# Optimization experiments

Measured on AMD Instinct MI355X. Metric: run time of the kernel, lower is better.

Reference implementation:

```python
import jax, jax.numpy as jnp
import numpy as np

B, N, T, F_IN, F_OUT = 4, 2048, 12, 32, 32
ALPHA = 0.2  # leaky relu negative slope
NEG_INF = -9e15


def setup_inputs() -> dict:
    key = jax.random.key(0)
    k = jax.random.split(key, 6)
    x = jax.random.normal(k[0], (B, N, T, F_IN), dtype=jnp.float32)
    adj = jax.random.randint(k[1], (N, N), 0, 2, dtype=jnp.int32)
    W = jax.random.normal(k[2], (T * F_IN, T * F_OUT), dtype=jnp.float32) * 0.05
    a = jax.random.normal(k[3], (2 * T * F_OUT, 1), dtype=jnp.float32) * 0.05
    conv_w = jax.random.normal(k[4], (T, T, 3), dtype=jnp.float32) * 0.1  # (out_ch, in_ch, k)
    conv_b = jnp.zeros((T,), dtype=jnp.float32)
    return {"x": x, "adj": adj, "W": W, "a": a, "conv_w": conv_w, "conv_b": conv_b}


def reference(x, adj, W, a, conv_w, conv_b):
    Bz, Nn, Tt, Fi = x.shape
    Fo = W.shape[1] // Tt
    # temporal conv: channels = timesteps, length = nodes*features
    xt = x.transpose(0, 2, 1, 3).reshape(Bz, Tt, Nn * Fi)  # (B,T,L)
    xt = jax.lax.conv_general_dilated(
        xt, conv_w, window_strides=(1,), padding=[(1, 1)],
        dimension_numbers=("NCH", "OIH", "NCH")) + conv_b[None, :, None]
    xt = xt.reshape(Bz, Tt, Nn, Fi).transpose(0, 2, 1, 3).reshape(Bz, Nn, Tt * Fi)
    Wh = xt @ W  # (B, N, T*Fo)
    # e[b,i,j] = leakyrelu(Wh[b,i].a1 + Wh[b,j].a2)  -- avoids O(N^2 * 2F) concat
    a1 = a[: Tt * Fo, 0]
    a2 = a[Tt * Fo:, 0]
    f1 = Wh @ a1  # (B, N)
    f2 = Wh @ a2  # (B, N)
    e = jax.nn.leaky_relu(f1[:, :, None] + f2[:, None, :], negative_slope=ALPHA)
    e = jnp.where(adj[None, :, :] > 0, e, NEG_INF)
    attn = jax.nn.softmax(e, axis=-1)  # (B, N, N); dropout omitted (eval mode)
    h_prime = attn @ Wh  # (B, N, T*Fo)
    return jax.nn.elu(h_prime).reshape(Bz, Nn, Tt, Fo)
```

## Files before the change

kernel.cpp:

```cpp
#include <hip/hip_runtime.h>

using short8 = __attribute__((ext_vector_type(8))) short;
using f32x4  = __attribute__((ext_vector_type(4))) float;
using f32x16 = __attribute__((ext_vector_type(16))) float;

__device__ __forceinline__ unsigned short f2bf(float f) {
  unsigned u = __float_as_uint(f);
  u += 0x7fffu + ((u >> 16) & 1u);
  return (unsigned short)(u >> 16);
}

__global__ __launch_bounds__(256) void pack_w_kernel(const float* __restrict__ W,
                                                     unsigned short* __restrict__ wtp) {
  const int f = blockIdx.x * 4 + (threadIdx.x >> 6);
  const int l = threadIdx.x & 63;
  const int kk = f / 24, ct = f % 24;
  const int il = l & 15, kg = l >> 4;
  const float* src = W + (size_t)(kk * 32 + kg * 8) * 384 + ct * 16 + il;
  short8 v;
#pragma unroll
  for (int e = 0; e < 8; ++e) v[e] = (short)f2bf(src[(size_t)e * 384]);
  *reinterpret_cast<short8*>((char*)wtp + ((size_t)f << 10) + l * 16) = v;
}

__global__ __launch_bounds__(256) void adjmask_kernel(const int* __restrict__ adj,
                                                      unsigned* __restrict__ adjm,
                                                      float* __restrict__ f12) {
  if (blockIdx.x < 64) f12[blockIdx.x * 256 + threadIdx.x] = 0.f;
  const int wv = (blockIdx.x << 2) + (threadIdx.x >> 6);
  const int lane = threadIdx.x & 63;
  const int row = wv >> 5, j0 = (wv & 31) << 6;
  unsigned long long mask = __ballot(adj[(size_t)row * 2048 + j0 + lane] > 0);
  if (lane == 0) {
    adjm[row * 64 + (j0 >> 5)]     = (unsigned)mask;
    adjm[row * 64 + (j0 >> 5) + 1] = (unsigned)(mask >> 32);
  }
}

__global__ __launch_bounds__(256) void gemm_wh5_kernel(const float* __restrict__ x,
                                                       const float* __restrict__ cw,
                                                       const float* __restrict__ cb,
                                                       const unsigned short* __restrict__ wtp,
                                                       const float* __restrict__ a,
                                                       unsigned short* __restrict__ whp,
                                                       float* __restrict__ f1,
                                                       float* __restrict__ f2) {
  __shared__ __align__(16) char lds[24768 + 6400 + 1792];
  float* xin = (float*)lds;
  unsigned short* atile = (unsigned short*)lds;
  unsigned short* wtile = (unsigned short*)(lds + 24768);
  float* cws = (float*)(lds + 24768 + 6400);
  float* cbs = cws + 432;

  const int tid = threadIdx.x;
  const int rb = blockIdx.x;
  const int b = rb >> 8;
  const int jg2 = (rb >> 1) & 127;
  const int ch2 = rb & 1;
  const int r0 = ((b << 7) + jg2) << 4;
  const int w = tid >> 6, lane = tid & 63;
  const int il = lane & 15, kg = lane >> 4;

  for (int i = tid; i < 432; i += 256) cws[i] = cw[i];
  if (tid < 12) cbs[tid] = cb[tid];
  const float* xb = x + (size_t)b * 2048 * 12 * 32;
#pragma unroll
  for (int t = 0; t < 12; ++t) {
    for (int i = tid; i < 514; i += 256) {
      const int gp = jg2 * 512 + i - 1;
      float v = 0.f;
      if ((unsigned)gp < 65536u) v = xb[((size_t)(gp >> 5) * 12 + t) * 32 + (gp & 31)];
      xin[t * 516 + i] = v;
    }
  }
  __syncthreads();

  const int ploc = tid * 2;
  float accv0[12], accv1[12];
#pragma unroll
  for (int to = 0; to < 12; ++to) { accv0[to] = cbs[to]; accv1[to] = cbs[to]; }
#pragma unroll
  for (int ti = 0; ti < 12; ++ti) {
    const float x0 = xin[ti * 516 + ploc];
    const float x1 = xin[ti * 516 + ploc + 1];
    const float x2 = xin[ti * 516 + ploc + 2];
    const float x3 = xin[ti * 516 + ploc + 3];
#pragma unroll
    for (int to = 0; to < 12; ++to) {
      const float* wp = &cws[(to * 12 + ti) * 3];
      const float w0 = wp[0], w1 = wp[1], w2 = wp[2];
      accv0[to] += x0 * w0 + x1 * w1 + x2 * w2;
      accv1[to] += x1 * w0 + x2 * w1 + x3 * w2;
    }
  }
  __syncthreads();

  {
    const int row = ploc >> 5, f = ploc & 31;
    unsigned* ap32 = (unsigned*)(atile + row * 392 + f);
#pragma unroll
    for (int to = 0; to < 12; ++to) {
      const unsigned lo = f2bf(accv0[to]), hi = f2bf(accv1[to]);
      ap32[to * 16] = lo | (hi << 16);
    }
  }
  __syncthreads();

  f32x4 acc[3];
#pragma unroll
  for (int t = 0; t < 3; ++t) acc[t] = (f32x4){0.f, 0.f, 0.f, 0.f};
  const unsigned short* arow = atile + il * 392 + kg * 8;
  const int ct0 = ch2 * 12 + w * 3;
  const char* wb = (const char*)wtp + ((size_t)ct0 << 10) + lane * 16;

  short8 bcur[3], bnxt[3];
#pragma unroll
  for (int t = 0; t < 3; ++t)
    bcur[t] = *reinterpret_cast<const short8*>(wb + ((size_t)t << 10));
#pragma unroll
  for (int kk = 0; kk < 12; ++kk) {
    if (kk < 11) {
#pragma unroll
      for (int t = 0; t < 3; ++t)
        bnxt[t] = *reinterpret_cast<const short8*>(wb + (((size_t)(kk + 1) * 24 + t) << 10));
    }
    short8 af = *reinterpret_cast<const short8*>(arow + kk * 32);
#pragma unroll
    for (int t = 0; t < 3; ++t)
      acc[t] = __builtin_amdgcn_mfma_f32_16x16x32_bf16(af, bcur[t], acc[t], 0, 0, 0);
#pragma unroll
    for (int t = 0; t < 3; ++t) bcur[t] = bnxt[t];
  }

  float p1[4] = {0.f, 0.f, 0.f, 0.f}, p2[4] = {0.f, 0.f, 0.f, 0.f};
#pragma unroll
  for (int t = 0; t < 3; ++t) {
    const int c = (ct0 + t) * 16 + il;
    const float a1v = a[c], a2v = a[384 + c];
#pragma unroll
    for (int r = 0; r < 4; ++r) { p1[r] += acc[t][r] * a1v; p2[r] += acc[t][r] * a2v; }
  }
#pragma unroll
  for (int off = 1; off < 16; off <<= 1) {
#pragma unroll
    for (int r = 0; r < 4; ++r) { p1[r] += __shfl_xor(p1[r], off); p2[r] += __shfl_xor(p2[r], off); }
  }
  if (il == 0) {
#pragma unroll
    for (int r = 0; r < 4; ++r) {
      atomicAdd(&f1[r0 + kg * 4 + r], p1[r]);
      atomicAdd(&f2[r0 + kg * 4 + r], p2[r]);
    }
  }
#pragma unroll
  for (int t = 0; t < 3; ++t)
#pragma unroll
    for (int r = 0; r < 4; ++r)
      wtile[(kg * 4 + r) * 200 + (w * 3 + t) * 16 + il] = f2bf(acc[t][r]);
  __syncthreads();

#pragma unroll
  for (int rep = 0; rep < 2; ++rep) {
    const int flat = rep * 256 + tid;
    if (flat < 384) {
      const int ct32l = flat >> 6, l = flat & 63;
      const int l5 = l & 31, hw2 = l >> 5;
      short8 v;
#pragma unroll
      for (int e = 0; e < 8; ++e)
        v[e] = (short)wtile[(hw2 * 8 + e) * 200 + ct32l * 32 + l5];
      const int ct32g = ch2 * 6 + ct32l;
      *reinterpret_cast<short8*>((char*)whp +
          ((((size_t)b * 128 + jg2) * 12 + ct32g) << 10) + l * 16) = v;
    }
  }
}

__global__ __launch_bounds__(256) void f2max_kernel(const float* __restrict__ f2,
                                                    float* __restrict__ gmax) {
  __shared__ float wm[4];
  const int b = blockIdx.x;
  const int tid = threadIdx.x;
  float m = -3.0e38f;
  for (int i = tid; i < 2048; i += 256) m = fmaxf(m, f2[b * 2048 + i]);
#pragma unroll
  for (int off = 32; off; off >>= 1) m = fmaxf(m, __shfl_xor(m, off));
  if ((tid & 63) == 0) wm[tid >> 6] = m;
  __syncthreads();
  if (tid == 0) gmax[b] = fmaxf(fmaxf(wm[0], wm[1]), fmaxf(wm[2], wm[3]));
}

__global__ __launch_bounds__(256, 3) void attn13_kernel(const float* __restrict__ f1,
                                                        const float* __restrict__ f2,
                                                        const unsigned* __restrict__ adjm,
                                                        const unsigned short* __restrict__ whp,
                                                        const float* __restrict__ gmax,
                                                        float* __restrict__ out) {
  __shared__ float red[4][32][64];
  __shared__ float dred[128];
  const int bi = blockIdx.x;
  const int combo = bi % 12;
  const int b  = combo & 3;
  const int ch = combo >> 2;
  const int i0 = (bi / 12) << 5;
  const int tid = threadIdx.x;
  const int ks = tid >> 6;
  const int lane = tid & 63;
  const int l5 = lane & 31, hw = lane >> 5;
  const int hw8 = hw * 8;
  const int ig = i0 + l5;

  const unsigned* adjr = adjm + (size_t)ig * 64 + ks * 16;
  const float* f2b = f2 + b * 2048 + ks * 512 + hw8;
  const char* pbase = (const char*)whp +
      ((((size_t)b * 128 + ks * 32) * 12 + ch * 4) << 10) + lane * 16;

  const float f1v = f1[b * 2048 + ig];
  const float gm = gmax[b];
  const float mz = f1v + gm;
  const float m  = fmaxf(mz, 0.2f * mz);
  const float Az = f1v - m;
  const float Bz = 0.2f * f1v - m;

  const f32x16 zero16 = {0.f,0.f,0.f,0.f,0.f,0.f,0.f,0.f,0.f,0.f,0.f,0.f,0.f,0.f,0.f,0.f};
  f32x16 acc[4];
#pragma unroll
  for (int t = 0; t < 4; ++t) acc[t] = zero16;
  float denom = 0.f;

  short8 bA[4], bB[4];
  float4 fA0, fA1, fB0, fB1;
  unsigned wC, wN;

#define LOADB(AR, KK)                                                                   \
  { _Pragma("unroll")                                                                   \
    for (int tt = 0; tt < 4; ++tt)                                                      \
      AR[tt] = *reinterpret_cast<const short8*>(pbase + (size_t)(KK) * 12288 +          \
                                                (size_t)tt * 1024); }

#define PEL(GV, BIT, DST)                                                               \
  { const float z_ = Az + (GV);                                                         \
    const float e_ = fmaxf(z_, fmaf((GV), 0.2f, Bz));                                   \
    DST = ((bits_ >> (BIT)) & 1u) ? __expf(e_) : 0.f; }

#define PKBF(HI, LO) (((__float_as_uint(HI) + 0x8000u) & 0xffff0000u) |                 \
                      ((__float_as_uint(LO) + 0x8000u) >> 16))

#define STEPD(AR, F0, F1, SH, KK, DL)                                                   \
  { const unsigned bits_ = wC >> ((SH) + hw8);                                          \
    float p0_, p1_, p2_, p3_, p4_, p5_, p6_, p7_;                                       \
    PEL(F0.x, 0, p0_)  PEL(F0.y, 1, p1_)  PEL(F0.z, 2, p2_)  PEL(F0.w, 3, p3_)          \
    PEL(F1.x, 4, p4_)  PEL(F1.y, 5, p5_)  PEL(F1.z, 6, p6_)  PEL(F1.w, 7, p7_)          \
    denom += (((p0_ + p1_) + (p2_ + p3_)) + ((p4_ + p5_) + (p6_ + p7_)));               \
    union { unsigned u[4]; short8 s8; } cc;                                             \
    cc.u[0] = PKBF(p1_, p0_); cc.u[1] = PKBF(p3_, p2_);                                 \
    cc.u[2] = PKBF(p5_, p4_); cc.u[3] = PKBF(p7_, p6_);                                 \
    _Pragma("unroll")                                                                   \
    for (int tt = 0; tt < 4; ++tt)                                                      \
      acc[tt] = __builtin_amdgcn_mfma_f32_32x32x16_bf16(cc.s8, AR[tt], acc[tt], 0, 0, 0); \
    if (DL) {                                                                           \
      LOADB(AR, (KK) + 2)                                                               \
      const float* fp_ = f2b + ((KK) + 2) * 16;                                         \
      F0 = *reinterpret_cast<const float4*>(fp_);                                       \
      F1 = *reinterpret_cast<const float4*>(fp_ + 4);                                   \
    } }

  LOADB(bA, 0) LOADB(bB, 1)
  fA0 = *reinterpret_cast<const float4*>(f2b);
  fA1 = *reinterpret_cast<const float4*>(f2b + 4);
  fB0 = *reinterpret_cast<const float4*>(f2b + 16);
  fB1 = *reinterpret_cast<const float4*>(f2b + 20);
  wC = adjr[0];
  wN = adjr[1];

  for (int t = 0; t < 16; ++t) {
    STEPD(bA, fA0, fA1, 0, 2 * t, (t < 15))
    STEPD(bB, fB0, fB1, 16, 2 * t + 1, (t < 15))
    wC = wN;
    wN = adjr[(t + 2 < 16) ? t + 2 : 15];
  }
#undef LOADB
#undef PEL
#undef PKBF
#undef STEPD

  float dn = denom + __shfl_xor(denom, 32);
  if (hw == 0) dred[ks * 32 + l5] = dn;

#pragma unroll
  for (int r = 0; r < 2; ++r) {
#pragma unroll
    for (int tt = 0; tt < 2; ++tt) {
#pragma unroll
      for (int q = 0; q < 16; ++q) {
        const int row = (q & 3) + 8 * (q >> 2) + 4 * hw;
        red[ks][row][tt * 32 + l5] = acc[r * 2 + tt][q];
      }
    }
    __syncthreads();
    const size_t ob = ((size_t)b * 2048 + i0) * 384 + ch * 128 + r * 64;
#pragma unroll
    for (int p = 0; p < 8; ++p) {
      const int idx = p * 256 + tid;
      const int row = idx >> 6;
      const int c = idx & 63;
      float v = red[0][row][c] + red[1][row][c] + red[2][row][c] + red[3][row][c];
      const float d = dred[row] + dred[32 + row] + dred[64 + row] + dred[96 + row];
      v /= d;
      v = v > 0.f ? v : expm1f(v);
      out[ob + (size_t)row * 384 + c] = v;
    }
    __syncthreads();
  }
}

extern "C" void kernel_launch(void* const* d_in, const int* in_sizes, int n_in,
                              void* d_out, int out_size, void* d_ws, size_t ws_size,
                              hipStream_t stream) {
  const float* x  = (const float*)d_in[0];
  const int* adj  = (const int*)d_in[1];
  const float* W  = (const float*)d_in[2];
  const float* a  = (const float*)d_in[3];
  const float* cw = (const float*)d_in[4];
  const float* cb = (const float*)d_in[5];
  float* out = (float*)d_out;

  char* ws = (char*)d_ws;
  unsigned short* wtp = (unsigned short*)ws; ws += (size_t)147456 * 2;
  unsigned short* whp = (unsigned short*)ws; ws += (size_t)3145728 * 2;
  float* f1           = (float*)ws;          ws += (size_t)8192 * 4;
  float* f2           = (float*)ws;          ws += (size_t)8192 * 4;
  unsigned* adjm      = (unsigned*)ws;       ws += (size_t)2048 * 64 * 4;
  float* gmax         = (float*)ws;          ws += 64;

  pack_w_kernel<<<dim3(72), 256, 0, stream>>>(W, wtp);
  adjmask_kernel<<<dim3(16384), 256, 0, stream>>>(adj, adjm, f1);
  gemm_wh5_kernel<<<dim3(1024), 256, 0, stream>>>(x, cw, cb, wtp, a, whp, f1, f2);
  f2max_kernel<<<dim3(4), 256, 0, stream>>>(f2, gmax);
  attn13_kernel<<<dim3(768), 256, 0, stream>>>(f1, f2, adjm, whp, gmax, out);
}
```

Before: 79.79 us.

## Split attention into probability-generation kernel and pure MFMA aggregation kernel

Attention probabilities were recomputed three times, once per channel chunk, inside the MFMA loop. They are now computed once by a new pgen kernel, which writes bf16 probabilities in MFMA operand layout to a 32 MB workspace and accumulates the row denominators with atomics. The aggregation kernel then only streams the P and Wh operands into MFMAs. This removes the redundant exp work and the ALU work interleaved with matrix ops, but adds a large extra HBM write and read of the P matrix plus one more kernel launch.

```diff
diff --git a/kernel.cpp b/kernel.cpp
--- a/kernel.cpp
+++ b/kernel.cpp
@@ -25,8 +25,10 @@
 
 __global__ __launch_bounds__(256) void adjmask_kernel(const int* __restrict__ adj,
                                                       unsigned* __restrict__ adjm,
-                                                      float* __restrict__ f12) {
+                                                      float* __restrict__ f12,
+                                                      float* __restrict__ dsum) {
   if (blockIdx.x < 64) f12[blockIdx.x * 256 + threadIdx.x] = 0.f;
+  else if (blockIdx.x < 96) dsum[(blockIdx.x - 64) * 256 + threadIdx.x] = 0.f;
   const int wv = (blockIdx.x << 2) + (threadIdx.x >> 6);
   const int lane = threadIdx.x & 63;
   const int row = wv >> 5, j0 = (wv & 31) << 6;
@@ -190,30 +192,24 @@
   if (tid == 0) gmax[b] = fmaxf(fmaxf(wm[0], wm[1]), fmaxf(wm[2], wm[3]));
 }
 
-__global__ __launch_bounds__(256, 3) void attn13_kernel(const float* __restrict__ f1,
-                                                        const float* __restrict__ f2,
-                                                        const unsigned* __restrict__ adjm,
-                                                        const unsigned short* __restrict__ whp,
-                                                        const float* __restrict__ gmax,
-                                                        float* __restrict__ out) {
-  __shared__ float red[4][32][64];
-  __shared__ float dred[128];
+__global__ __launch_bounds__(256) void pgen_kernel(const float* __restrict__ f1,
+                                                   const float* __restrict__ f2,
+                                                   const unsigned* __restrict__ adjm,
+                                                   const float* __restrict__ gmax,
+                                                   unsigned short* __restrict__ php,
+                                                   float* __restrict__ dsum) {
+  __shared__ float ds[32];
   const int bi = blockIdx.x;
-  const int combo = bi % 12;
-  const int b  = combo & 3;
-  const int ch = combo >> 2;
-  const int i0 = (bi / 12) << 5;
+  const int b = bi >> 9;
+  const int rg = (bi >> 3) & 63;
+  const int jc = bi & 7;
   const int tid = threadIdx.x;
-  const int ks = tid >> 6;
-  const int lane = tid & 63;
+  const int wv = tid >> 6, lane = tid & 63;
   const int l5 = lane & 31, hw = lane >> 5;
   const int hw8 = hw * 8;
-  const int ig = i0 + l5;
-
-  const unsigned* adjr = adjm + (size_t)ig * 64 + ks * 16;
-  const float* f2b = f2 + b * 2048 + ks * 512 + hw8;
-  const char* pbase = (const char*)whp +
-      ((((size_t)b * 128 + ks * 32) * 12 + ch * 4) << 10) + lane * 16;
+  const int ig = rg * 32 + l5;
+  if (tid < 32) ds[tid] = 0.f;
+  __syncthreads();
 
   const float f1v = f1[b * 2048 + ig];
   const float gm = gmax[b];
@@ -221,72 +217,86 @@
   const float m  = fmaxf(mz, 0.2f * mz);
   const float Az = f1v - m;
   const float Bz = 0.2f * f1v - m;
+  const float* f2b = f2 + b * 2048;
+  const unsigned* adjrow = adjm + (size_t)ig * 64;
+  char* phpb = (char*)php + ((((size_t)b * 64 + rg) * 128) << 10) + lane * 16;
+
+  float dloc = 0.f;
+#pragma unroll
+  for (int s = 0; s < 4; ++s) {
+    const int js = jc * 16 + wv * 4 + s;
+    const int j0 = js * 16;
+    const float* fp = f2b + j0 + hw8;
+    const float4 g0 = *reinterpret_cast<const float4*>(fp);
+    const float4 g1 = *reinterpret_cast<const float4*>(fp + 4);
+    const unsigned word = adjrow[j0 >> 5];
+    const unsigned bits = word >> ((j0 & 16) + hw8);
+    const float gv[8] = {g0.x, g0.y, g0.z, g0.w, g1.x, g1.y, g1.z, g1.w};
+    union { unsigned short s[8]; short8 s8; } v;
+#pragma unroll
+    for (int e = 0; e < 8; ++e) {
+      const float z = Az + gv[e];
+      const float ee = fmaxf(z, fmaf(gv[e], 0.2f, Bz));
+      const float p = ((bits >> e) & 1u) ? __expf(ee) : 0.f;
+      dloc += p;
+      v.s[e] = (unsigned short)((__float_as_uint(p) + 0x8000u) >> 16);
+    }
+    *reinterpret_cast<short8*>(phpb + ((size_t)js << 10)) = v.s8;
+  }
+  atomicAdd(&ds[l5], dloc);
+  __syncthreads();
+  if (tid < 32) atomicAdd(&dsum[b * 2048 + rg * 32 + tid], ds[tid]);
+}
+
+__global__ __launch_bounds__(256, 3) void attn14_kernel(const unsigned short* __restrict__ php,
+                                                        const unsigned short* __restrict__ whp,
+                                                        const float* __restrict__ dsum,
+                                                        float* __restrict__ out) {
+  __shared__ float red[4][32][64];
+  const int bi = blockIdx.x;
+  const int combo = bi % 12;
+  const int b  = combo & 3;
+  const int ch = combo >> 2;
+  const int rg = bi / 12;
+  const int i0 = rg << 5;
+  const int tid = threadIdx.x;
+  const int ks = tid >> 6;
+  const int lane = tid & 63;
+  const int l5 = lane & 31, hw = lane >> 5;
+
+  const char* abase = (const char*)php +
+      ((((size_t)b * 64 + rg) * 128 + ks * 32) << 10) + lane * 16;
+  const char* pbase = (const char*)whp +
+      ((((size_t)b * 128 + ks * 32) * 12 + ch * 4) << 10) + lane * 16;
 
   const f32x16 zero16 = {0.f,0.f,0.f,0.f,0.f,0.f,0.f,0.f,0.f,0.f,0.f,0.f,0.f,0.f,0.f,0.f};
   f32x16 acc[4];
 #pragma unroll
   for (int t = 0; t < 4; ++t) acc[t] = zero16;
-  float denom = 0.f;
-
-  short8 bA[4], bB[4];
-  float4 fA0, fA1, fB0, fB1;
-  unsigned wC, wN;
-
-#define LOADB(AR, KK)                                                                   \
-  { _Pragma("unroll")                                                                   \
-    for (int tt = 0; tt < 4; ++tt)                                                      \
-      AR[tt] = *reinterpret_cast<const short8*>(pbase + (size_t)(KK) * 12288 +          \
-                                                (size_t)tt * 1024); }
-
-#define PEL(GV, BIT, DST)                                                               \
-  { const float z_ = Az + (GV);                                                         \
-    const float e_ = fmaxf(z_, fmaf((GV), 0.2f, Bz));                                   \
-    DST = ((bits_ >> (BIT)) & 1u) ? __expf(e_) : 0.f; }
-
-#define PKBF(HI, LO) (((__float_as_uint(HI) + 0x8000u) & 0xffff0000u) |                 \
-                      ((__float_as_uint(LO) + 0x8000u) >> 16))
-
-#define STEPD(AR, F0, F1, SH, KK, DL)                                                   \
-  { const unsigned bits_ = wC >> ((SH) + hw8);                                          \
-    float p0_, p1_, p2_, p3_, p4_, p5_, p6_, p7_;                                       \
-    PEL(F0.x, 0, p0_)  PEL(F0.y, 1, p1_)  PEL(F0.z, 2, p2_)  PEL(F0.w, 3, p3_)          \
-    PEL(F1.x, 4, p4_)  PEL(F1.y, 5, p5_)  PEL(F1.z, 6, p6_)  PEL(F1.w, 7, p7_)          \
-    denom += (((p0_ + p1_) + (p2_ + p3_)) + ((p4_ + p5_) + (p6_ + p7_)));               \
-    union { unsigned u[4]; short8 s8; } cc;                                             \
-    cc.u[0] = PKBF(p1_, p0_); cc.u[1] = PKBF(p3_, p2_);                                 \
-    cc.u[2] = PKBF(p5_, p4_); cc.u[3] = PKBF(p7_, p6_);                                 \
+
+  short8 aA, aB, bA[4], bB[4];
+
+#define LOADAB(AS, BR, KK)                                                              \
+  { AS = *reinterpret_cast<const short8*>(abase + ((size_t)(KK) << 10));                \
     _Pragma("unroll")                                                                   \
     for (int tt = 0; tt < 4; ++tt)                                                      \
-      acc[tt] = __builtin_amdgcn_mfma_f32_32x32x16_bf16(cc.s8, AR[tt], acc[tt], 0, 0, 0); \
-    if (DL) {                                                                           \
-      LOADB(AR, (KK) + 2)                                                               \
-      const float* fp_ = f2b + ((KK) + 2) * 16;                                         \
-      F0 = *reinterpret_cast<const float4*>(fp_);                                       \
-      F1 = *reinterpret_cast<const float4*>(fp_ + 4);                                   \
-    } }
-
-  LOADB(bA, 0) LOADB(bB, 1)
-  fA0 = *reinterpret_cast<const float4*>(f2b);
-  fA1 = *reinterpret_cast<const float4*>(f2b + 4);
-  fB0 = *reinterpret_cast<const float4*>(f2b + 16);
-  fB1 = *reinterpret_cast<const float4*>(f2b + 20);
-  wC = adjr[0];
-  wN = adjr[1];
-
+      BR[tt] = *reinterpret_cast<const short8*>(pbase + (size_t)(KK) * 12288 +          \
+                                                (size_t)tt * 1024); }
+
+  LOADAB(aA, bA, 0) LOADAB(aB, bB, 1)
   for (int t = 0; t < 16; ++t) {
-    STEPD(bA, fA0, fA1, 0, 2 * t, (t < 15))
-    STEPD(bB, fB0, fB1, 16, 2 * t + 1, (t < 15))
-    wC = wN;
-    wN = adjr[(t + 2 < 16) ? t + 2 : 15];
-  }
-#undef LOADB
-#undef PEL
-#undef PKBF
-#undef STEPD
-
-  float dn = denom + __shfl_xor(denom, 32);
-  if (hw == 0) dred[ks * 32 + l5] = dn;
-
+#pragma unroll
+    for (int tt = 0; tt < 4; ++tt)
+      acc[tt] = __builtin_amdgcn_mfma_f32_32x32x16_bf16(aA, bA[tt], acc[tt], 0, 0, 0);
+    if (t < 15) LOADAB(aA, bA, 2 * t + 2)
+#pragma unroll
+    for (int tt = 0; tt < 4; ++tt)
+      acc[tt] = __builtin_amdgcn_mfma_f32_32x32x16_bf16(aB, bB[tt], acc[tt], 0, 0, 0);
+    if (t < 15) LOADAB(aB, bB, 2 * t + 3)
+  }
+#undef LOADAB
+
+  const float* dsb = dsum + b * 2048 + i0;
 #pragma unroll
   for (int r = 0; r < 2; ++r) {
 #pragma unroll
@@ -305,8 +315,7 @@
       const int row = idx >> 6;
       const int c = idx & 63;
       float v = red[0][row][c] + red[1][row][c] + red[2][row][c] + red[3][row][c];
-      const float d = dred[row] + dred[32 + row] + dred[64 + row] + dred[96 + row];
-      v /= d;
+      v /= dsb[row];
       v = v > 0.f ? v : expm1f(v);
       out[ob + (size_t)row * 384 + c] = v;
     }
@@ -328,14 +337,17 @@
   char* ws = (char*)d_ws;
   unsigned short* wtp = (unsigned short*)ws; ws += (size_t)147456 * 2;
   unsigned short* whp = (unsigned short*)ws; ws += (size_t)3145728 * 2;
+  unsigned short* php = (unsigned short*)ws; ws += (size_t)16777216 * 2;
   float* f1           = (float*)ws;          ws += (size_t)8192 * 4;
   float* f2           = (float*)ws;          ws += (size_t)8192 * 4;
+  float* dsum         = (float*)ws;          ws += (size_t)8192 * 4;
   unsigned* adjm      = (unsigned*)ws;       ws += (size_t)2048 * 64 * 4;
   float* gmax         = (float*)ws;          ws += 64;
 
   pack_w_kernel<<<dim3(72), 256, 0, stream>>>(W, wtp);
-  adjmask_kernel<<<dim3(16384), 256, 0, stream>>>(adj, adjm, f1);
+  adjmask_kernel<<<dim3(16384), 256, 0, stream>>>(adj, adjm, f1, dsum);
   gemm_wh5_kernel<<<dim3(1024), 256, 0, stream>>>(x, cw, cb, wtp, a, whp, f1, f2);
   f2max_kernel<<<dim3(4), 256, 0, stream>>>(f2, gmax);
-  attn13_kernel<<<dim3(768), 256, 0, stream>>>(f1, f2, adjm, whp, gmax, out);
-}
+  pgen_kernel<<<dim3(2048), 256, 0, stream>>>(f1, f2, adjm, gmax, php, dsum);
+  attn14_kernel<<<dim3(768), 256, 0, stream>>>(php, whp, dsum, out);
+}
```

Result: slower. 83.90 us (+5.1%).

## Factor attention exponentials into per-node tables and restructure attention with LDS-staged P

Applied to the files above, without the earlier changes.

Rewrites exp(leakyrelu(f1+f2)-m) as a product of per-row and per-column exponentials, with the per-column exp(f2) and exp(0.2*f2) precomputed once as packed bf16 in f2max_kernel. This removes the per-element exp from the attention inner loop. The attention kernel now uses 512-thread blocks, each covering all output channels for 32 rows, and 16x16x32 MFMAs whose P operand is staged through double-buffered LDS. The Wh pack layout in the GEMM epilogue is reshaped to match. This avoids the cross-wave split-K reduction but adds a barrier per step, bf16 rounding of the exp table, and a branch selection per element.

```diff
diff --git a/kernel.cpp b/kernel.cpp
--- a/kernel.cpp
+++ b/kernel.cpp
@@ -2,7 +2,6 @@
 
 using short8 = __attribute__((ext_vector_type(8))) short;
 using f32x4  = __attribute__((ext_vector_type(4))) float;
-using f32x16 = __attribute__((ext_vector_type(16))) float;
 
 __device__ __forceinline__ unsigned short f2bf(float f) {
   unsigned u = __float_as_uint(f);
@@ -159,30 +158,42 @@
       wtile[(kg * 4 + r) * 200 + (w * 3 + t) * 16 + il] = f2bf(acc[t][r]);
   __syncthreads();
 
+  const int js = jg2 >> 1;
+  const int lbase = (jg2 & 1) * 32;
 #pragma unroll
   for (int rep = 0; rep < 2; ++rep) {
     const int flat = rep * 256 + tid;
     if (flat < 384) {
-      const int ct32l = flat >> 6, l = flat & 63;
-      const int l5 = l & 31, hw2 = l >> 5;
+      const int ctl = flat >> 5;
+      const int ll = flat & 31;
+      const int l_g = lbase + ll;
       short8 v;
 #pragma unroll
-      for (int e = 0; e < 8; ++e)
-        v[e] = (short)wtile[(hw2 * 8 + e) * 200 + ct32l * 32 + l5];
-      const int ct32g = ch2 * 6 + ct32l;
+      for (int e = 0; e < 8; ++e) {
+        const int jrow = (ll >> 4) * 8 + e;
+        v[e] = (short)wtile[jrow * 200 + ctl * 16 + (ll & 15)];
+      }
+      const int ctg = ch2 * 12 + ctl;
       *reinterpret_cast<short8*>((char*)whp +
-          ((((size_t)b * 128 + jg2) * 12 + ct32g) << 10) + l * 16) = v;
+          ((((size_t)b * 64 + js) * 24 + ctg) << 10) + l_g * 16) = v;
     }
   }
 }
 
 __global__ __launch_bounds__(256) void f2max_kernel(const float* __restrict__ f2,
-                                                    float* __restrict__ gmax) {
+                                                    float* __restrict__ gmax,
+                                                    unsigned* __restrict__ etab) {
   __shared__ float wm[4];
   const int b = blockIdx.x;
   const int tid = threadIdx.x;
   float m = -3.0e38f;
-  for (int i = tid; i < 2048; i += 256) m = fmaxf(m, f2[b * 2048 + i]);
+  for (int i = tid; i < 2048; i += 256) {
+    const float v = f2[b * 2048 + i];
+    m = fmaxf(m, v);
+    const unsigned e2 = f2bf(__expf(v));
+    const unsigned q2 = f2bf(__expf(0.2f * v));
+    etab[b * 2048 + i] = (e2 << 16) | q2;
+  }
 #pragma unroll
   for (int off = 32; off; off >>= 1) m = fmaxf(m, __shfl_xor(m, off));
   if ((tid & 63) == 0) wm[tid >> 6] = m;
@@ -190,127 +201,112 @@
   if (tid == 0) gmax[b] = fmaxf(fmaxf(wm[0], wm[1]), fmaxf(wm[2], wm[3]));
 }
 
-__global__ __launch_bounds__(256, 3) void attn13_kernel(const float* __restrict__ f1,
-                                                        const float* __restrict__ f2,
+__global__ __launch_bounds__(512, 4) void attn15_kernel(const float* __restrict__ f1,
+                                                        const unsigned* __restrict__ etab,
                                                         const unsigned* __restrict__ adjm,
                                                         const unsigned short* __restrict__ whp,
                                                         const float* __restrict__ gmax,
                                                         float* __restrict__ out) {
-  __shared__ float red[4][32][64];
-  __shared__ float dred[128];
+  __shared__ __align__(16) char plds[4096 + 128];
+  float* drows = (float*)(plds + 4096);
   const int bi = blockIdx.x;
-  const int combo = bi % 12;
-  const int b  = combo & 3;
-  const int ch = combo >> 2;
-  const int i0 = (bi / 12) << 5;
+  const int b = bi >> 6, rg = bi & 63;
   const int tid = threadIdx.x;
-  const int ks = tid >> 6;
-  const int lane = tid & 63;
-  const int l5 = lane & 31, hw = lane >> 5;
-  const int hw8 = hw * 8;
-  const int ig = i0 + l5;
-
-  const unsigned* adjr = adjm + (size_t)ig * 64 + ks * 16;
-  const float* f2b = f2 + b * 2048 + ks * 512 + hw8;
-  const char* pbase = (const char*)whp +
-      ((((size_t)b * 128 + ks * 32) * 12 + ch * 4) << 10) + lane * 16;
-
-  const float f1v = f1[b * 2048 + ig];
+  const int w = tid >> 6, lam = tid & 63;
+  const int h = tid >> 8;
+  const int q = w & 3;
+  const int mrem = tid & 255;
+  const int lp = mrem >> 2, pair = mrem & 3;
+  const int rowp = h * 16 + (lp & 15);
+  const int igp = rg * 32 + rowp;
+  const int jin = (lp >> 4) * 8 + pair * 2;
+
+  if (tid < 32) drows[tid] = 0.f;
+
+  const float f1v = f1[b * 2048 + igp];
   const float gm = gmax[b];
   const float mz = f1v + gm;
-  const float m  = fmaxf(mz, 0.2f * mz);
-  const float Az = f1v - m;
-  const float Bz = 0.2f * f1v - m;
-
-  const f32x16 zero16 = {0.f,0.f,0.f,0.f,0.f,0.f,0.f,0.f,0.f,0.f,0.f,0.f,0.f,0.f,0.f,0.f};
-  f32x16 acc[4];
-#pragma unroll
-  for (int t = 0; t < 4; ++t) acc[t] = zero16;
-  float denom = 0.f;
-
-  short8 bA[4], bB[4];
-  float4 fA0, fA1, fB0, fB1;
-  unsigned wC, wN;
-
-#define LOADB(AR, KK)                                                                   \
+  const float mm = fmaxf(mz, 0.2f * mz);
+  const float E1 = __expf(f1v - mm);
+  const float F1 = __expf(0.2f * f1v - mm);
+  const float T  = __expf(-f1v);
+  const unsigned* adjr = adjm + (size_t)igp * 64;
+  const unsigned* etb = etab + b * 2048;
+  char* pwr = plds + h * 1024 + lp * 16 + pair * 4;
+  const char* prd = plds + h * 1024 + lam * 16;
+  const char* wbase = (const char*)whp + ((((size_t)b * 64) * 24 + q * 6) << 10) + lam * 16;
+
+  float dloc = 0.f;
+  f32x4 acc[6];
+#pragma unroll
+  for (int t = 0; t < 6; ++t) acc[t] = (f32x4){0.f, 0.f, 0.f, 0.f};
+
+#define PGEN(BUF, S)                                                                    \
+  { const unsigned bits_ = adjr[S] >> jin;                                              \
+    const uint2 tt_ = *reinterpret_cast<const uint2*>(etb + (S) * 32 + jin);            \
+    const float e2a_ = __uint_as_float(tt_.x & 0xffff0000u);                            \
+    const float q2a_ = __uint_as_float(tt_.x << 16);                                    \
+    const bool pa_ = e2a_ > T;                                                          \
+    float va_ = (pa_ ? e2a_ : q2a_) * (pa_ ? E1 : F1);                                  \
+    va_ = (bits_ & 1u) ? va_ : 0.f;                                                     \
+    const float e2b_ = __uint_as_float(tt_.y & 0xffff0000u);                            \
+    const float q2b_ = __uint_as_float(tt_.y << 16);                                    \
+    const bool pb_ = e2b_ > T;                                                          \
+    float vb_ = (pb_ ? e2b_ : q2b_) * (pb_ ? E1 : F1);                                  \
+    vb_ = (bits_ & 2u) ? vb_ : 0.f;                                                     \
+    dloc += va_ + vb_;                                                                  \
+    const unsigned pk_ = ((__float_as_uint(vb_) + 0x8000u) & 0xffff0000u) |             \
+                         ((__float_as_uint(va_) + 0x8000u) >> 16);                      \
+    *reinterpret_cast<unsigned*>(pwr + (BUF) * 2048) = pk_; }
+
+#define LOADB(AR, S)                                                                    \
   { _Pragma("unroll")                                                                   \
-    for (int tt = 0; tt < 4; ++tt)                                                      \
-      AR[tt] = *reinterpret_cast<const short8*>(pbase + (size_t)(KK) * 12288 +          \
-                                                (size_t)tt * 1024); }
-
-#define PEL(GV, BIT, DST)                                                               \
-  { const float z_ = Az + (GV);                                                         \
-    const float e_ = fmaxf(z_, fmaf((GV), 0.2f, Bz));                                   \
-    DST = ((bits_ >> (BIT)) & 1u) ? __expf(e_) : 0.f; }
-
-#define PKBF(HI, LO) (((__float_as_uint(HI) + 0x8000u) & 0xffff0000u) |                 \
-                      ((__float_as_uint(LO) + 0x8000u) >> 16))
-
-#define STEPD(AR, F0, F1, SH, KK, DL)                                                   \
-  { const unsigned bits_ = wC >> ((SH) + hw8);                                          \
-    float p0_, p1_, p2_, p3_, p4_, p5_, p6_, p7_;                                       \
-    PEL(F0.x, 0, p0_)  PEL(F0.y, 1, p1_)  PEL(F0.z, 2, p2_)  PEL(F0.w, 3, p3_)          \
-    PEL(F1.x, 4, p4_)  PEL(F1.y, 5, p5_)  PEL(F1.z, 6, p6_)  PEL(F1.w, 7, p7_)          \
-    denom += (((p0_ + p1_) + (p2_ + p3_)) + ((p4_ + p5_) + (p6_ + p7_)));               \
-    union { unsigned u[4]; short8 s8; } cc;                                             \
-    cc.u[0] = PKBF(p1_, p0_); cc.u[1] = PKBF(p3_, p2_);                                 \
-    cc.u[2] = PKBF(p5_, p4_); cc.u[3] = PKBF(p7_, p6_);                                 \
-    _Pragma("unroll")                                                                   \
-    for (int tt = 0; tt < 4; ++tt)                                                      \
-      acc[tt] = __builtin_amdgcn_mfma_f32_32x32x16_bf16(cc.s8, AR[tt], acc[tt], 0, 0, 0); \
-    if (DL) {                                                                           \
-      LOADB(AR, (KK) + 2)                                                               \
-      const float* fp_ = f2b + ((KK) + 2) * 16;                                         \
-      F0 = *reinterpret_cast<const float4*>(fp_);                                       \
-      F1 = *reinterpret_cast<const float4*>(fp_ + 4);                                   \
-    } }
-
+    for (int tt = 0; tt < 6; ++tt)                                                      \
+      AR[tt] = *reinterpret_cast<const short8*>(wbase + (((size_t)(S) * 24 + tt) << 10)); }
+
+  short8 bA[6], bB[6];
+  PGEN(0, 0)
   LOADB(bA, 0) LOADB(bB, 1)
-  fA0 = *reinterpret_cast<const float4*>(f2b);
-  fA1 = *reinterpret_cast<const float4*>(f2b + 4);
-  fB0 = *reinterpret_cast<const float4*>(f2b + 16);
-  fB1 = *reinterpret_cast<const float4*>(f2b + 20);
-  wC = adjr[0];
-  wN = adjr[1];
-
-  for (int t = 0; t < 16; ++t) {
-    STEPD(bA, fA0, fA1, 0, 2 * t, (t < 15))
-    STEPD(bB, fB0, fB1, 16, 2 * t + 1, (t < 15))
-    wC = wN;
-    wN = adjr[(t + 2 < 16) ? t + 2 : 15];
-  }
+  __syncthreads();
+
+  for (int s = 0; s < 64; s += 2) {
+    {
+      short8 aF = *reinterpret_cast<const short8*>(prd);
+      PGEN(1, s + 1)
+#pragma unroll
+      for (int tt = 0; tt < 6; ++tt)
+        acc[tt] = __builtin_amdgcn_mfma_f32_16x16x32_bf16(aF, bA[tt], acc[tt], 0, 0, 0);
+      if (s + 2 < 64) LOADB(bA, s + 2)
+      __syncthreads();
+    }
+    {
+      short8 aG = *reinterpret_cast<const short8*>(prd + 2048);
+      if (s + 2 < 64) PGEN(0, s + 2)
+#pragma unroll
+      for (int tt = 0; tt < 6; ++tt)
+        acc[tt] = __builtin_amdgcn_mfma_f32_16x16x32_bf16(aG, bB[tt], acc[tt], 0, 0, 0);
+      if (s + 3 < 64) LOADB(bB, s + 3)
+      __syncthreads();
+    }
+  }
+#undef PGEN
 #undef LOADB
-#undef PEL
-#undef PKBF
-#undef STEPD
-
-  float dn = denom + __shfl_xor(denom, 32);
-  if (hw == 0) dred[ks * 32 + l5] = dn;
-
-#pragma unroll
-  for (int r = 0; r < 2; ++r) {
-#pragma unroll
-    for (int tt = 0; tt < 2; ++tt) {
-#pragma unroll
-      for (int q = 0; q < 16; ++q) {
-        const int row = (q & 3) + 8 * (q >> 2) + 4 * hw;
-        red[ks][row][tt * 32 + l5] = acc[r * 2 + tt][q];
-      }
-    }
-    __syncthreads();
-    const size_t ob = ((size_t)b * 2048 + i0) * 384 + ch * 128 + r * 64;
-#pragma unroll
-    for (int p = 0; p < 8; ++p) {
-      const int idx = p * 256 + tid;
-      const int row = idx >> 6;
-      const int c = idx & 63;
-      float v = red[0][row][c] + red[1][row][c] + red[2][row][c] + red[3][row][c];
-      const float d = dred[row] + dred[32 + row] + dred[64 + row] + dred[96 + row];
-      v /= d;
+
+  dloc += __shfl_xor(dloc, 1);
+  dloc += __shfl_xor(dloc, 2);
+  if ((lam & 3) == 0) atomicAdd(&drows[rowp], dloc);
+  __syncthreads();
+
+  const size_t ob = ((size_t)b * 2048 + rg * 32) * 384 + q * 96;
+#pragma unroll
+  for (int tt = 0; tt < 6; ++tt) {
+#pragma unroll
+    for (int r = 0; r < 4; ++r) {
+      const int row = h * 16 + (lam >> 4) * 4 + r;
+      float v = acc[tt][r] / drows[row];
       v = v > 0.f ? v : expm1f(v);
-      out[ob + (size_t)row * 384 + c] = v;
-    }
-    __syncthreads();
+      out[ob + (size_t)row * 384 + tt * 16 + (lam & 15)] = v;
+    }
   }
 }
 
@@ -332,10 +328,11 @@
   float* f2           = (float*)ws;          ws += (size_t)8192 * 4;
   unsigned* adjm      = (unsigned*)ws;       ws += (size_t)2048 * 64 * 4;
   float* gmax         = (float*)ws;          ws += 64;
+  unsigned* etab      = (unsigned*)ws;       ws += (size_t)8192 * 4;
 
   pack_w_kernel<<<dim3(72), 256, 0, stream>>>(W, wtp);
   adjmask_kernel<<<dim3(16384), 256, 0, stream>>>(adj, adjm, f1);
   gemm_wh5_kernel<<<dim3(1024), 256, 0, stream>>>(x, cw, cb, wtp, a, whp, f1, f2);
-  f2max_kernel<<<dim3(4), 256, 0, stream>>>(f2, gmax);
-  attn13_kernel<<<dim3(768), 256, 0, stream>>>(f1, f2, adjm, whp, gmax, out);
-}
+  f2max_kernel<<<dim3(4), 256, 0, stream>>>(f2, gmax, etab);
+  attn15_kernel<<<dim3(256), 512, 0, stream>>>(f1, etab, adjm, whp, gmax, out);
+}
```

Result: slower. 102.1 us (+27.9%).

## Factor attention exponentials into per-row and per-column terms with precomputed table

Applied to the files above, without the earlier changes.

Splits exp(leakyrelu(f1+f2)-m) into a per-row factor (exp(f1-m) or exp(0.2f1-m)) times a per-column factor (exp(f2) or exp(0.2f2)). The column factors are precomputed once per batch as a packed bf16 pair table in the f2max kernel. The branch is chosen by comparing exp(f2) against exp(-f1). This removes the N^2 transcendental exp calls from the attention inner loop and leaves a select and a multiply. In exchange the column factors are rounded to bf16 and exp(f2) may overflow or lose precision for large f2 values.

```diff
diff --git a/kernel.cpp b/kernel.cpp
--- a/kernel.cpp
+++ b/kernel.cpp
@@ -177,12 +177,19 @@
 }
 
 __global__ __launch_bounds__(256) void f2max_kernel(const float* __restrict__ f2,
-                                                    float* __restrict__ gmax) {
+                                                    float* __restrict__ gmax,
+                                                    unsigned* __restrict__ etab) {
   __shared__ float wm[4];
   const int b = blockIdx.x;
   const int tid = threadIdx.x;
   float m = -3.0e38f;
-  for (int i = tid; i < 2048; i += 256) m = fmaxf(m, f2[b * 2048 + i]);
+  for (int i = tid; i < 2048; i += 256) {
+    const float v = f2[b * 2048 + i];
+    m = fmaxf(m, v);
+    const unsigned e2 = f2bf(__expf(v));
+    const unsigned q2 = f2bf(__expf(0.2f * v));
+    etab[b * 2048 + i] = (e2 << 16) | q2;
+  }
 #pragma unroll
   for (int off = 32; off; off >>= 1) m = fmaxf(m, __shfl_xor(m, off));
   if ((tid & 63) == 0) wm[tid >> 6] = m;
@@ -190,8 +197,8 @@
   if (tid == 0) gmax[b] = fmaxf(fmaxf(wm[0], wm[1]), fmaxf(wm[2], wm[3]));
 }
 
-__global__ __launch_bounds__(256, 3) void attn13_kernel(const float* __restrict__ f1,
-                                                        const float* __restrict__ f2,
+__global__ __launch_bounds__(256, 3) void attn16_kernel(const float* __restrict__ f1,
+                                                        const unsigned* __restrict__ etab,
                                                         const unsigned* __restrict__ adjm,
                                                         const unsigned short* __restrict__ whp,
                                                         const float* __restrict__ gmax,
@@ -211,7 +218,7 @@
   const int ig = i0 + l5;
 
   const unsigned* adjr = adjm + (size_t)ig * 64 + ks * 16;
-  const float* f2b = f2 + b * 2048 + ks * 512 + hw8;
+  const unsigned* etb = etab + b * 2048 + ks * 512 + hw8;
   const char* pbase = (const char*)whp +
       ((((size_t)b * 128 + ks * 32) * 12 + ch * 4) << 10) + lane * 16;
 
@@ -219,8 +226,9 @@
   const float gm = gmax[b];
   const float mz = f1v + gm;
   const float m  = fmaxf(mz, 0.2f * mz);
-  const float Az = f1v - m;
-  const float Bz = 0.2f * f1v - m;
+  const float E1 = __expf(f1v - m);
+  const float F1 = __expf(0.2f * f1v - m);
+  const float T  = __expf(-f1v);
 
   const f32x16 zero16 = {0.f,0.f,0.f,0.f,0.f,0.f,0.f,0.f,0.f,0.f,0.f,0.f,0.f,0.f,0.f,0.f};
   f32x16 acc[4];
@@ -229,7 +237,7 @@
   float denom = 0.f;
 
   short8 bA[4], bB[4];
-  float4 fA0, fA1, fB0, fB1;
+  uint4 eA0, eA1, eB0, eB1;
   unsigned wC, wN;
 
 #define LOADB(AR, KK)                                                                   \
@@ -238,19 +246,21 @@
       AR[tt] = *reinterpret_cast<const short8*>(pbase + (size_t)(KK) * 12288 +          \
                                                 (size_t)tt * 1024); }
 
-#define PEL(GV, BIT, DST)                                                               \
-  { const float z_ = Az + (GV);                                                         \
-    const float e_ = fmaxf(z_, fmaf((GV), 0.2f, Bz));                                   \
-    DST = ((bits_ >> (BIT)) & 1u) ? __expf(e_) : 0.f; }
+#define PELE(UW, BIT, DST)                                                              \
+  { const float e2_ = __uint_as_float((UW) & 0xffff0000u);                              \
+    const float q2_ = __uint_as_float((UW) << 16);                                      \
+    const bool p_ = e2_ > T;                                                            \
+    const float v_ = (p_ ? e2_ : q2_) * (p_ ? E1 : F1);                                 \
+    DST = ((bits_ >> (BIT)) & 1u) ? v_ : 0.f; }
 
 #define PKBF(HI, LO) (((__float_as_uint(HI) + 0x8000u) & 0xffff0000u) |                 \
                       ((__float_as_uint(LO) + 0x8000u) >> 16))
 
-#define STEPD(AR, F0, F1, SH, KK, DL)                                                   \
+#define STEPD(AR, T0, T1, SH, KK, DL)                                                   \
   { const unsigned bits_ = wC >> ((SH) + hw8);                                          \
     float p0_, p1_, p2_, p3_, p4_, p5_, p6_, p7_;                                       \
-    PEL(F0.x, 0, p0_)  PEL(F0.y, 1, p1_)  PEL(F0.z, 2, p2_)  PEL(F0.w, 3, p3_)          \
-    PEL(F1.x, 4, p4_)  PEL(F1.y, 5, p5_)  PEL(F1.z, 6, p6_)  PEL(F1.w, 7, p7_)          \
+    PELE(T0.x, 0, p0_)  PELE(T0.y, 1, p1_)  PELE(T0.z, 2, p2_)  PELE(T0.w, 3, p3_)      \
+    PELE(T1.x, 4, p4_)  PELE(T1.y, 5, p5_)  PELE(T1.z, 6, p6_)  PELE(T1.w, 7, p7_)      \
     denom += (((p0_ + p1_) + (p2_ + p3_)) + ((p4_ + p5_) + (p6_ + p7_)));               \
     union { unsigned u[4]; short8 s8; } cc;                                             \
     cc.u[0] = PKBF(p1_, p0_); cc.u[1] = PKBF(p3_, p2_);                                 \
@@ -260,27 +270,27 @@
       acc[tt] = __builtin_amdgcn_mfma_f32_32x32x16_bf16(cc.s8, AR[tt], acc[tt], 0, 0, 0); \
     if (DL) {                                                                           \
       LOADB(AR, (KK) + 2)                                                               \
-      const float* fp_ = f2b + ((KK) + 2) * 16;                                         \
-      F0 = *reinterpret_cast<const float4*>(fp_);                                       \
-      F1 = *reinterpret_cast<const float4*>(fp_ + 4);                                   \
+      const unsigned* ep_ = etb + ((KK) + 2) * 16;                                      \
+      T0 = *reinterpret_cast<const uint4*>(ep_);                                        \
+      T1 = *reinterpret_cast<const uint4*>(ep_ + 4);                                    \
     } }
 
   LOADB(bA, 0) LOADB(bB, 1)
-  fA0 = *reinterpret_cast<const float4*>(f2b);
-  fA1 = *reinterpret_cast<const float4*>(f2b + 4);
-  fB0 = *reinterpret_cast<const float4*>(f2b + 16);
-  fB1 = *reinterpret_cast<const float4*>(f2b + 20);
+  eA0 = *reinterpret_cast<const uint4*>(etb);
+  eA1 = *reinterpret_cast<const uint4*>(etb + 4);
+  eB0 = *reinterpret_cast<const uint4*>(etb + 16);
+  eB1 = *reinterpret_cast<const uint4*>(etb + 20);
   wC = adjr[0];
   wN = adjr[1];
 
   for (int t = 0; t < 16; ++t) {
-    STEPD(bA, fA0, fA1, 0, 2 * t, (t < 15))
-    STEPD(bB, fB0, fB1, 16, 2 * t + 1, (t < 15))
+    STEPD(bA, eA0, eA1, 0, 2 * t, (t < 15))
+    STEPD(bB, eB0, eB1, 16, 2 * t + 1, (t < 15))
     wC = wN;
     wN = adjr[(t + 2 < 16) ? t + 2 : 15];
   }
 #undef LOADB
-#undef PEL
+#undef PELE
 #undef PKBF
 #undef STEPD
 
@@ -332,10 +342,11 @@
   float* f2           = (float*)ws;          ws += (size_t)8192 * 4;
   unsigned* adjm      = (unsigned*)ws;       ws += (size_t)2048 * 64 * 4;
   float* gmax         = (float*)ws;          ws += 64;
+  unsigned* etab      = (unsigned*)ws;       ws += (size_t)8192 * 4;
 
   pack_w_kernel<<<dim3(72), 256, 0, stream>>>(W, wtp);
   adjmask_kernel<<<dim3(16384), 256, 0, stream>>>(adj, adjm, f1);
   gemm_wh5_kernel<<<dim3(1024), 256, 0, stream>>>(x, cw, cb, wtp, a, whp, f1, f2);
-  f2max_kernel<<<dim3(4), 256, 0, stream>>>(f2, gmax);
-  attn13_kernel<<<dim3(768), 256, 0, stream>>>(f1, f2, adjm, whp, gmax, out);
-}
+  f2max_kernel<<<dim3(4), 256, 0, stream>>>(f2, gmax, etab);
+  attn16_kernel<<<dim3(768), 256, 0, stream>>>(f1, etab, adjm, whp, gmax, out);
+}
```

Result: no change. 79.53 us (-0.3%).
